# Optimization experiments

Measured on AMD Instinct MI355X. Metric: run time of the kernel, lower is better.

Reference implementation:

```python
import jax, jax.numpy as jnp
import numpy as np

B = 32768   # batch
D0 = 64     # node-0 feature dim
D1 = 64     # node-1 feature dim
M = 8       # modules per node
H = 256     # hidden width
O0 = 128    # node-0 output width
O1 = 32     # final output width
B_INIT = 0.1
INIT_W = 0.003


def _fanin_uniform(key, shape):
    bound = 1.0 / np.sqrt(shape[-2])
    return jax.random.uniform(key, shape, jnp.float32, -bound, bound)


def setup_inputs() -> dict:
    key = jax.random.key(0)
    ks = jax.random.split(key, 10)
    feat = jax.random.normal(ks[0], (B, D0 + D1), jnp.float32)
    a0 = jax.random.randint(ks[1], (B,), 0, M)
    a1 = jax.random.randint(ks[2], (B,), 0, M)
    oh0 = jax.nn.one_hot(a0, M, dtype=jnp.float32)
    oh1 = jax.nn.one_hot(a1, M, dtype=jnp.float32)
    input_val = jnp.concatenate([feat, oh0, oh1], axis=1)  # [B, 144]
    # node 0 (all post-interface, hidden init + ReLU on both layers since graph_depth < last)
    W00 = _fanin_uniform(ks[3], (M, D0, H)); b00 = jnp.full((M, H), B_INIT, jnp.float32)
    W01 = _fanin_uniform(ks[4], (M, H, O0)); b01 = jnp.full((M, O0), B_INIT, jnp.float32)
    # node 1 pre-interface (layer i=0)
    W1p = _fanin_uniform(ks[5], (M, D1, H)); b1p = jnp.full((M, H), B_INIT, jnp.float32)
    # node 1 post-interface layer i=1: input = node0_out (128) concat pre (256) = 384
    W1a = _fanin_uniform(ks[6], (M, O0 + H, O0)); b1a = jnp.full((M, O0), B_INIT, jnp.float32)
    # node 1 output layer i=2: uniform(-init_w, init_w), Identity activation
    W1o = jax.random.uniform(ks[7], (M, O0, O1), jnp.float32, -INIT_W, INIT_W)
    b1o = jax.random.uniform(ks[8], (M, O1), jnp.float32, -INIT_W, INIT_W)
    return {"input_val": input_val, "W00": W00, "b00": b00, "W01": W01, "b01": b01,
            "W1p": W1p, "b1p": b1p, "W1a": W1a, "b1a": b1a, "W1o": W1o, "b1o": b1o}


def _routed(x, W, b, onehot, act):
    # per-module linear for all modules, then one-hot select the assigned module per sample
    y = jnp.einsum('bi,mio->bmo', x, W) + b          # [B, M, out]
    y = jnp.einsum('bmo,bm->bo', y, onehot)           # [B, out]
    return jax.nn.relu(y) if act else y


def reference(input_val, W00, b00, W01, b01, W1p, b1p, W1a, b1a, W1o, b1o):
    feat0 = input_val[:, :D0]
    feat1 = input_val[:, D0:D0 + D1]
    oh0 = input_val[:, D0 + D1:D0 + D1 + M]
    oh1 = input_val[:, D0 + D1 + M:D0 + D1 + 2 * M]
    # graph depth 0, node 0: post-interface MLP (ReLU on both layers)
    h = _routed(feat0, W00, b00, oh0, True)
    h = _routed(h, W01, b01, oh0, True)               # [B, O0]
    # graph depth 1, node 1: pre-interface, concat prev-depth output, post-interface
    g = _routed(feat1, W1p, b1p, oh1, True)           # [B, H]
    g = _routed(jnp.concatenate([h, g], axis=-1), W1a, b1a, oh1, True)  # [B, O0]
    out = _routed(g, W1o, b1o, oh1, False)            # [B, O1], Identity output activation
    return out
```

## Files before the change

kernel.cpp:

```cpp
#include <hip/hip_runtime.h>
#include <hip/hip_bf16.h>

#define BATCH 32768
#define NPAIR 64
#define NBLK  128

typedef __bf16 bf16x8 __attribute__((ext_vector_type(8)));
typedef float  f32x4  __attribute__((ext_vector_type(4)));
typedef float  f32x4e __attribute__((ext_vector_type(4)));
static_assert(sizeof(bf16x8) == 16, "bf16x8 must be 16B");

#define WS_CNT      0
#define WS_BASE     256
#define WS_BH       1024
#define WS_PAIR     66560
#define WS_ROWLIST  197632
#define WS_WF00     336896
#define WS_WF01     599040
#define WS_WF1P     1123328
#define WS_WF1A     1385472
#define WS_WF1O     2171904

__device__ __forceinline__ unsigned short f2bf(float x) {
  __bf16 h = (__bf16)x;
  return __builtin_bit_cast(unsigned short, h);
}

#define KEEP(x) asm volatile("" : "+v"(x))

__global__ __launch_bounds__(256) void k_combo(const float* __restrict__ w00,
                                               const float* __restrict__ w01,
                                               const float* __restrict__ w1p,
                                               const float* __restrict__ w1a,
                                               const float* __restrict__ w1o,
                                               const float* __restrict__ inp,
                                               char* __restrict__ ws) {
  __shared__ unsigned short lds[64 * 72];
  int bid = blockIdx.x;
  if (bid >= 240) {
    int* h = (int*)lds;
    int rbid = bid - 240;
    int t = threadIdx.x;
    if (t < NPAIR) h[t] = 0;
    __syncthreads();
    int r = rbid * 256 + t;
    const float* q = inp + (size_t)r * 144 + 128;
    float4 u0 = *(const float4*)(q + 0);
    float4 u1 = *(const float4*)(q + 4);
    float4 v0 = *(const float4*)(q + 8);
    float4 v1 = *(const float4*)(q + 12);
    int a0 = 0;
    if (u0.y > 0.5f) a0 = 1; if (u0.z > 0.5f) a0 = 2; if (u0.w > 0.5f) a0 = 3;
    if (u1.x > 0.5f) a0 = 4; if (u1.y > 0.5f) a0 = 5; if (u1.z > 0.5f) a0 = 6; if (u1.w > 0.5f) a0 = 7;
    int a1 = 0;
    if (v0.y > 0.5f) a1 = 1; if (v0.z > 0.5f) a1 = 2; if (v0.w > 0.5f) a1 = 3;
    if (v1.x > 0.5f) a1 = 4; if (v1.y > 0.5f) a1 = 5; if (v1.z > 0.5f) a1 = 6; if (v1.w > 0.5f) a1 = 7;
    int p = a0 * 8 + a1;
    ((int*)(ws + WS_PAIR))[r] = p;
    atomicAdd(&h[p], 1);
    __syncthreads();
    if (t < NPAIR) ((int*)(ws + WS_BH))[rbid * NPAIR + t] = h[t];
    return;
  }
  const float* src; char* dst; int I, O, lt, NT, KC;
  if (bid < 32)       { src = w00; dst = ws + WS_WF00; I = 64;  O = 256; lt = bid;       NT = 16; KC = 2; }
  else if (bid < 96)  { src = w01; dst = ws + WS_WF01; I = 256; O = 128; lt = bid - 32;  NT = 8;  KC = 8; }
  else if (bid < 128) { src = w1p; dst = ws + WS_WF1P; I = 64;  O = 256; lt = bid - 96;  NT = 16; KC = 2; }
  else if (bid < 224) { src = w1a; dst = ws + WS_WF1A; I = 384; O = 128; lt = bid - 128; NT = 8;  KC = 12; }
  else                { src = w1o; dst = ws + WS_WF1O; I = 128; O = 32;  lt = bid - 224; NT = 2;  KC = 4; }
  int tI = I >> 6;
  int tO = (O + 63) >> 6;
  int m   = lt / (tI * tO);
  int rem = lt % (tI * tO);
  int ib = rem / tO, ob = rem % tO;
  int tx = threadIdx.x & 63, ty = threadIdx.x >> 6;
  const float* s = src + (size_t)m * I * O;
  #pragma unroll 4
  for (int s4 = 0; s4 < 16; ++s4) {
    int li = s4 * 4 + ty;
    int o  = ob * 64 + tx;
    float v = (o < O) ? s[(size_t)(ib * 64 + li) * O + o] : 0.f;
    lds[li * 72 + tx] = f2bf(v);
  }
  __syncthreads();
  int lane = threadIdx.x & 63, u = threadIdx.x >> 6;
  int ln = lane & 15, lq = lane >> 4;
  #pragma unroll
  for (int it = 0; it < 2; ++it) {
    int fi  = it * 4 + u;
    int ntl = fi >> 1, kcl = fi & 1;
    int ntg = ob * 4 + ntl, kcg = ib * 2 + kcl;
    if (ntg * 16 < O) {
      bf16x8 f;
      #pragma unroll
      for (int j = 0; j < 8; ++j)
        f[j] = __builtin_bit_cast(__bf16, lds[(kcl * 32 + lq * 8 + j) * 72 + ntl * 16 + ln]);
      *(bf16x8*)(dst + (((size_t)(m * NT + ntg) * KC + kcg) * 64 + lane) * 16) = f;
    }
  }
}

__global__ __launch_bounds__(256) void k_part(const int* __restrict__ bh,
                                              const int* __restrict__ pairArr,
                                              int* __restrict__ cnt,
                                              int* __restrict__ base,
                                              int* __restrict__ rowlist) {
  __shared__ int lbh[NBLK * NPAIR];
  __shared__ int loff[NPAIR];
  __shared__ int h[NPAIR];
  int tid = threadIdx.x, bid = blockIdx.x;
  const int4* s4 = (const int4*)bh;
  int4* d4 = (int4*)lbh;
  #pragma unroll
  for (int i = 0; i < 8; ++i) d4[tid + i * 256] = s4[tid + i * 256];
  if (tid < NPAIR) h[tid] = 0;
  __syncthreads();
  if (tid < NPAIR) {
    int c = 0, partial = 0;
    for (int b = 0; b < NBLK; ++b) {
      int v = lbh[b * NPAIR + tid];
      if (b < bid) partial += v;
      c += v;
    }
    int ntp = (c + 31) >> 5;
    int z = ntp;
    #pragma unroll
    for (int d = 1; d < 64; d <<= 1) { int y = __shfl_up(z, d); if (tid >= d) z += y; }
    int pbase = (z - ntp) * 32;
    loff[tid] = pbase + partial;
    if (bid == 0) { cnt[tid] = c; base[tid] = pbase; }
  }
  __syncthreads();
  int r = bid * 256 + tid;
  int p = pairArr[r];
  int rank = atomicAdd(&h[p], 1);
  rowlist[loff[p] + rank] = r;
}

__global__ __launch_bounds__(512, 1) void k_fused(
    const float* __restrict__ inp,
    const float* __restrict__ b00, const float* __restrict__ b01,
    const float* __restrict__ b1p, const float* __restrict__ b1a,
    const float* __restrict__ b1o,
    const char* __restrict__ ws, float* __restrict__ out)
{
  __shared__ char smem[155648];
  unsigned short* G   = (unsigned short*)(smem + 98304);
  unsigned short* H1m = (unsigned short*)(smem + 114688);
  unsigned short* HO  = (unsigned short*)(smem + 131072);
  unsigned short* G2  = (unsigned short*)(smem + 139264);
  char*           xs  = smem + 147456;

  int p     = blockIdx.x >> 2;
  int slice = blockIdx.x & 3;
  int e0 = p >> 3, e1 = p & 7;
  int cnt = ((const int*)(ws + WS_CNT))[p];
  int pbase = ((const int*)(ws + WS_BASE))[p];
  int ntp = (cnt + 31) >> 5;
  if (slice >= ntp) return;
  const int* rlbase = (const int*)(ws + WS_ROWLIST) + pbase;

  int tid  = threadIdx.x;
  {
    const f32x4e* s1 = (const f32x4e*)(ws + WS_WF1A + (size_t)e1 * 98304);
    f32x4e* d1 = (f32x4e*)smem;
    #pragma unroll
    for (int i = 0; i < 12; ++i) d1[tid + i * 512] = s1[tid + i * 512];
  }

  int lane = tid & 63;
  int w    = tid >> 6;
  int ln = lane & 15, lq = lane >> 4;
  int kcol = lq * 8;

  bf16x8 w00f[2][2], w1pf[2][2];
  #pragma unroll
  for (int nt = 0; nt < 2; ++nt)
    #pragma unroll
    for (int kc = 0; kc < 2; ++kc) {
      w00f[nt][kc] = *(const bf16x8*)(ws + WS_WF00 + (size_t)e0 * 32768 +
                                      ((((w * 2 + nt) * 2 + kc) * 64 + lane) << 4));
      w1pf[nt][kc] = *(const bf16x8*)(ws + WS_WF1P + (size_t)e1 * 32768 +
                                      ((((w * 2 + nt) * 2 + kc) * 64 + lane) << 4));
    }
  bf16x8 wc[8];
  #pragma unroll
  for (int kc = 0; kc < 8; ++kc)
    wc[kc] = *(const bf16x8*)(ws + WS_WF01 + (size_t)e0 * 65536 +
                              (((w * 8 + kc) * 64 + lane) << 4));
  #pragma unroll
  for (int nt = 0; nt < 2; ++nt)
    #pragma unroll
    for (int kc = 0; kc < 2; ++kc) { KEEP(w00f[nt][kc]); KEEP(w1pf[nt][kc]); }
  #pragma unroll
  for (int kc = 0; kc < 8; ++kc) KEEP(wc[kc]);

  float bias00[2], bias1p[2];
  #pragma unroll
  for (int nt = 0; nt < 2; ++nt) {
    bias00[nt] = b00[e0 * 256 + w * 32 + nt * 16 + ln];
    bias1p[nt] = b1p[e1 * 256 + w * 32 + nt * 16 + ln];
  }
  float bias01 = b01[e0 * 128 + w * 16 + ln];
  float bias1a = b1a[e1 * 128 + w * 16 + ln];
  float bias1o = (w < 4) ? b1o[e1 * 32 + (w >> 1) * 16 + ln] : 0.f;

  const f32x4 z4 = {0.f, 0.f, 0.f, 0.f};
  int srow = tid >> 5, scol = tid & 31;
  __syncthreads();

  for (int t = slice; t < ntp; t += 4) {
    int nr = min(32, cnt - t * 32);
    const int* rl = rlbase + t * 32;

    #pragma unroll
    for (int pass = 0; pass < 2; ++pass) {
      int row = pass * 16 + srow;
      int rg = (row < nr) ? rl[row] : -1;
      ushort4 v8 = {0, 0, 0, 0};
      if (rg >= 0) {
        f32x4e u = __builtin_nontemporal_load(
            (const f32x4e*)(inp + (size_t)rg * 144 + scol * 4));
        v8.x = f2bf(u.x); v8.y = f2bf(u.y); v8.z = f2bf(u.z); v8.w = f2bf(u.w);
      }
      int byte = (row * 256 + scol * 8) ^ ((row & 7) << 4);
      *(ushort4*)(xs + byte) = v8;
    }
    __syncthreads();

    bf16x8 axf[2][2][2];
    #pragma unroll
    for (int half = 0; half < 2; ++half)
      #pragma unroll
      for (int mt = 0; mt < 2; ++mt)
        #pragma unroll
        for (int kc = 0; kc < 2; ++kc) {
          int row = mt * 16 + ln;
          int byte = (row * 256 + half * 128 + kc * 64 + lq * 16) ^ ((row & 7) << 4);
          axf[half][mt][kc] = *(const bf16x8*)(xs + byte);
        }
    #pragma unroll
    for (int nt = 0; nt < 2; ++nt) {
      int n = w * 32 + nt * 16 + ln;
      f32x4 acc0[2] = {z4, z4}, acc1[2] = {z4, z4};
      #pragma unroll
      for (int kc = 0; kc < 2; ++kc)
        #pragma unroll
        for (int mt = 0; mt < 2; ++mt) {
          acc0[mt] = __builtin_amdgcn_mfma_f32_16x16x32_bf16(axf[0][mt][kc], w00f[nt][kc], acc0[mt], 0, 0, 0);
          acc1[mt] = __builtin_amdgcn_mfma_f32_16x16x32_bf16(axf[1][mt][kc], w1pf[nt][kc], acc1[mt], 0, 0, 0);
        }
      #pragma unroll
      for (int mt = 0; mt < 2; ++mt)
        #pragma unroll
        for (int r = 0; r < 4; ++r) {
          int row = mt * 16 + lq * 4 + r;
          int sw = ((n << 1) ^ ((row & 7) << 4));
          H1m[(row * 512 + sw) >> 1] = f2bf(fmaxf(acc0[mt][r] + bias00[nt], 0.f));
          G  [(row * 512 + sw) >> 1] = f2bf(fmaxf(acc1[mt][r] + bias1p[nt], 0.f));
        }
    }
    __syncthreads();

    {
      f32x4 acc[2] = {z4, z4};
      #pragma unroll
      for (int kc = 0; kc < 8; ++kc) {
        #pragma unroll
        for (int mt = 0; mt < 2; ++mt) {
          int row = mt * 16 + ln;
          bf16x8 afr = *(const bf16x8*)&H1m[(row * 512 + (((kc * 32 + kcol) << 1) ^ ((row & 7) << 4))) >> 1];
          acc[mt] = __builtin_amdgcn_mfma_f32_16x16x32_bf16(afr, wc[kc], acc[mt], 0, 0, 0);
        }
      }
      int n = w * 16 + ln;
      #pragma unroll
      for (int mt = 0; mt < 2; ++mt)
        #pragma unroll
        for (int r = 0; r < 4; ++r) {
          int row = mt * 16 + lq * 4 + r;
          float v = fmaxf(acc[mt][r] + bias01, 0.f);
          HO[(row * 256 + ((n << 1) ^ ((row & 7) << 4))) >> 1] = f2bf(v);
        }
    }
    __syncthreads();

    {
      f32x4 acc1a[2] = {z4, z4};
      #pragma unroll
      for (int kc = 0; kc < 12; ++kc) {
        bf16x8 bfr = *(const bf16x8*)(smem + (((w * 12 + kc) * 64 + lane) << 4));
        #pragma unroll
        for (int mt = 0; mt < 2; ++mt) {
          bf16x8 afr;
          int row = mt * 16 + ln;
          if (kc < 4)
            afr = *(const bf16x8*)&HO[(row * 256 + (((kc * 32 + kcol) << 1) ^ ((row & 7) << 4))) >> 1];
          else {
            int kk = kc - 4;
            afr = *(const bf16x8*)&G[(row * 512 + (((kk * 32 + kcol) << 1) ^ ((row & 7) << 4))) >> 1];
          }
          acc1a[mt] = __builtin_amdgcn_mfma_f32_16x16x32_bf16(afr, bfr, acc1a[mt], 0, 0, 0);
        }
      }
      int n = w * 16 + ln;
      #pragma unroll
      for (int mt = 0; mt < 2; ++mt)
        #pragma unroll
        for (int r = 0; r < 4; ++r) {
          int row = mt * 16 + lq * 4 + r;
          float v = fmaxf(acc1a[mt][r] + bias1a, 0.f);
          G2[(row * 256 + ((n << 1) ^ ((row & 7) << 4))) >> 1] = f2bf(v);
        }
    }
    __syncthreads();

    if (w < 4) {
      int mt = w & 1;
      int n  = (w >> 1) * 16 + ln;
      f32x4 acc = z4;
      #pragma unroll
      for (int kc = 0; kc < 4; ++kc) {
        int row = mt * 16 + ln;
        bf16x8 afr = *(const bf16x8*)&G2[(row * 256 + (((kc * 32 + kcol) << 1) ^ ((row & 7) << 4))) >> 1];
        bf16x8 bfr = *(const bf16x8*)(ws + WS_WF1O + (size_t)e1 * 8192 +
                                      ((((w >> 1) * 4 + kc) * 64 + lane) << 4));
        acc = __builtin_amdgcn_mfma_f32_16x16x32_bf16(afr, bfr, acc, 0, 0, 0);
      }
      #pragma unroll
      for (int r = 0; r < 4; ++r) {
        int row = mt * 16 + lq * 4 + r;
        if (row < nr) {
          int rg = rl[row];
          __builtin_nontemporal_store(acc[r] + bias1o, &out[(size_t)rg * 32 + n]);
        }
      }
    }
  }
}

extern "C" void kernel_launch(void* const* d_in, const int* in_sizes, int n_in,
                              void* d_out, int out_size, void* d_ws, size_t ws_size,
                              hipStream_t stream) {
  const float* inp = (const float*)d_in[0];
  const float* w00 = (const float*)d_in[1];
  const float* b00 = (const float*)d_in[2];
  const float* w01 = (const float*)d_in[3];
  const float* b01 = (const float*)d_in[4];
  const float* w1p = (const float*)d_in[5];
  const float* b1p = (const float*)d_in[6];
  const float* w1a = (const float*)d_in[7];
  const float* b1a = (const float*)d_in[8];
  const float* w1o = (const float*)d_in[9];
  const float* b1o = (const float*)d_in[10];
  char*  ws  = (char*)d_ws;
  float* out = (float*)d_out;

  k_combo<<<368, 256, 0, stream>>>(w00, w01, w1p, w1a, w1o, inp, ws);
  k_part<<<NBLK, 256, 0, stream>>>((const int*)(ws + WS_BH),
                                   (const int*)(ws + WS_PAIR),
                                   (int*)(ws + WS_CNT), (int*)(ws + WS_BASE),
                                   (int*)(ws + WS_ROWLIST));
  k_fused<<<256, 512, 0, stream>>>(inp, b00, b01, b1p, b1a, b1o, ws, out);
}
```

Baseline: 48.53 us.

## Prefetch next tile's input rows into registers while computing current tile

Issues the global loads for the next 32-row tile before the first-layer MFMAs of the current tile, then converts and writes them to the shared staging buffer after the post-layer-1 barrier. This hides global-load latency behind compute and removes one barrier per iteration. It adds register pressure from the prefetch buffer, and correctness depends on the staging buffer no longer being read after that barrier.

```diff
diff --git a/kernel.cpp b/kernel.cpp
--- a/kernel.cpp
+++ b/kernel.cpp
@@ -207,16 +207,14 @@
 
   const f32x4 z4 = {0.f, 0.f, 0.f, 0.f};
   int srow = tid >> 5, scol = tid & 31;
-  __syncthreads();
-
-  for (int t = slice; t < ntp; t += 4) {
-    int nr = min(32, cnt - t * 32);
-    const int* rl = rlbase + t * 32;
-
+
+  {
+    int nr0 = min(32, cnt - slice * 32);
+    const int* rl0 = rlbase + slice * 32;
     #pragma unroll
     for (int pass = 0; pass < 2; ++pass) {
       int row = pass * 16 + srow;
-      int rg = (row < nr) ? rl[row] : -1;
+      int rg = (row < nr0) ? rl0[row] : -1;
       ushort4 v8 = {0, 0, 0, 0};
       if (rg >= 0) {
         f32x4e u = __builtin_nontemporal_load(
@@ -226,7 +224,31 @@
       int byte = (row * 256 + scol * 8) ^ ((row & 7) << 4);
       *(ushort4*)(xs + byte) = v8;
     }
-    __syncthreads();
+  }
+  __syncthreads();
+
+  for (int t = slice; t < ntp; t += 4) {
+    int nr = min(32, cnt - t * 32);
+    const int* rl = rlbase + t * 32;
+
+    int t2 = t + 4;
+    bool hasNext = (t2 < ntp);
+    f32x4e pre[2];
+    #pragma unroll
+    for (int pass = 0; pass < 2; ++pass) { pre[pass].x = 0; pre[pass].y = 0; pre[pass].z = 0; pre[pass].w = 0; }
+    if (hasNext) {
+      int nr2 = min(32, cnt - t2 * 32);
+      const int* rl2 = rlbase + t2 * 32;
+      #pragma unroll
+      for (int pass = 0; pass < 2; ++pass) {
+        int row = pass * 16 + srow;
+        int rg = (row < nr2) ? rl2[row] : -1;
+        if (rg >= 0)
+          pre[pass] = __builtin_nontemporal_load(
+              (const f32x4e*)(inp + (size_t)rg * 144 + scol * 4));
+      }
+      KEEP(pre[0]); KEEP(pre[1]);
+    }
 
     bf16x8 axf[2][2][2];
     #pragma unroll
@@ -261,6 +283,18 @@
         }
     }
     __syncthreads();
+
+    if (hasNext) {
+      #pragma unroll
+      for (int pass = 0; pass < 2; ++pass) {
+        int row = pass * 16 + srow;
+        ushort4 v8;
+        v8.x = f2bf(pre[pass].x); v8.y = f2bf(pre[pass].y);
+        v8.z = f2bf(pre[pass].z); v8.w = f2bf(pre[pass].w);
+        int byte = (row * 256 + scol * 8) ^ ((row & 7) << 4);
+        *(ushort4*)(xs + byte) = v8;
+      }
+    }
 
     {
       f32x4 acc[2] = {z4, z4};
```

New measurement: 45.30 us. -6.6%, faster.
